# Performance work log

Measured on AMD Instinct MI355X. Metric: run time of the kernel, lower is better.

The kernel has to match this reference:

```python
import jax, jax.numpy as jnp
import numpy as np

C, H, G = 64, 8, 8
EPS = 1e-5


def setup_inputs() -> dict:
    key = jax.random.key(0)
    k1, k2, k3 = jax.random.split(key, 3)
    x = jax.random.normal(k1, (1, C, 16, 16, 16), dtype=jnp.float32)
    gn_weight = jnp.ones((C,), dtype=jnp.float32)
    gn_bias = jnp.zeros((C,), dtype=jnp.float32)
    qkv_w = jax.random.normal(k2, (3 * C, C), dtype=jnp.float32) * (C ** -0.5)
    out_w = jax.random.normal(k3, (C, C), dtype=jnp.float32) * (C ** -0.5)
    out_b = jnp.zeros((C,), dtype=jnp.float32)
    return {"x": x, "gn_weight": gn_weight, "gn_bias": gn_bias,
            "qkv_w": qkv_w, "out_w": out_w, "out_b": out_b}


def reference(x, gn_weight, gn_bias, qkv_w, out_w, out_b):
    B, Cc, X, Y, Z = x.shape
    D = Cc // H                     # head_dim
    S = X * Y * Z                   # flattened spatial length
    scale = D ** -0.5

    # GroupNorm over (C//G, X, Y, Z) per group
    xg = x.reshape(B, G, Cc // G, X, Y, Z)
    mu = xg.mean(axis=(2, 3, 4, 5), keepdims=True)
    var = xg.var(axis=(2, 3, 4, 5), keepdims=True)
    xn = ((xg - mu) * jax.lax.rsqrt(var + EPS)).reshape(B, Cc, X, Y, Z)
    xn = xn * gn_weight[None, :, None, None, None] + gn_bias[None, :, None, None, None]

    # 1x1x1 conv == channel matmul
    qkv = jnp.einsum('oc,bcxyz->boxyz', qkv_w, xn)
    q, k, v = jnp.split(qkv, 3, axis=1)            # each [B, C, X, Y, Z]
    q = q.reshape(B, H, D, S)
    k = k.reshape(B, H, D, S)
    v = v.reshape(B, H, D, S)

    scores = jnp.einsum('bhds,bhdt->bhst', q, k) * scale   # [B,H,S,S]
    probs = jax.nn.softmax(scores, axis=-1)
    out = jnp.einsum('bhst,bhdt->bhds', probs, v)          # [B,H,D,S]
    out = out.reshape(B, Cc, X, Y, Z)

    out = jnp.einsum('oc,bcxyz->boxyz', out_w, out) + out_b[None, :, None, None, None]
    return out + x
```

## Files before the change

kernel.cpp:

```cpp
#include <hip/hip_runtime.h>
#include <math.h>

#define S 4096
#define EPS 1e-5f

#if __has_builtin(__builtin_amdgcn_exp2f)
#define EXP2F(x) __builtin_amdgcn_exp2f(x)
#else
#define EXP2F(x) exp2f(x)
#endif

#define WS_PSUM 0
#define WS_PSQ  64
#define WS_ATT  16384
#define QT_B 1310720
#define KT_B 1835008
#define VB_B 2359296

typedef _Float16 h8_t __attribute__((ext_vector_type(8)));
typedef _Float16 h4_t __attribute__((ext_vector_type(4)));
typedef __fp16   fp16v2 __attribute__((ext_vector_type(2)));
typedef float    f4_t __attribute__((ext_vector_type(4)));

union H8 { h8_t h; int4 v; int i[4]; };
union H4 { h4_t h; int2 v; int i[2]; };

static __device__ __forceinline__ int pkrtz(float a, float b) {
    fp16v2 p = __builtin_amdgcn_cvt_pkrtz(a, b);
    union { fp16v2 h; int i; } u; u.h = p; return u.i;
}

__global__ __launch_bounds__(256) void k_gnstat1(const float* __restrict__ x,
                                                 float* __restrict__ ws) {
    int b = blockIdx.x;
    int tid = threadIdx.x;
    const float4* p = (const float4*)(x + b * 4096);
    float s = 0.f, sq = 0.f;
    #pragma unroll
    for (int i = 0; i < 4; ++i) {
        float4 v = p[tid + i * 256];
        s  += v.x + v.y + v.z + v.w;
        sq += v.x * v.x + v.y * v.y + v.z * v.z + v.w * v.w;
    }
    #pragma unroll
    for (int m = 32; m >= 1; m >>= 1) {
        s  += __shfl_xor(s, m);
        sq += __shfl_xor(sq, m);
    }
    __shared__ float ls[4], lq[4];
    int w = tid >> 6;
    if ((tid & 63) == 0) { ls[w] = s; lq[w] = sq; }
    __syncthreads();
    if (tid == 0) {
        ws[WS_PSUM + b] = ls[0] + ls[1] + ls[2] + ls[3];
        ws[WS_PSQ  + b] = lq[0] + lq[1] + lq[2] + lq[3];
    }
}

__global__ __launch_bounds__(256) void k_qkv(const float* __restrict__ x,
                                             const float* __restrict__ qkvw,
                                             const float* __restrict__ gnw,
                                             const float* __restrict__ gnb,
                                             float* __restrict__ ws) {
    __shared__ float la[64], lb2[64], lw[512], lbias[8];
    int tid = threadIdx.x;
    int o0 = blockIdx.y * 8;
    int s = blockIdx.x * 256 + tid;

    if (tid < 64) {
        float sm = ws[WS_PSUM + tid];
        float sq = ws[WS_PSQ + tid];
        #pragma unroll
        for (int m = 1; m < 8; m <<= 1) {
            sm += __shfl_xor(sm, m);
            sq += __shfl_xor(sq, m);
        }
        const float inv_n = 1.0f / 32768.0f;
        float mu  = sm * inv_n;
        float var = sq * inv_n - mu * mu;
        float rs  = rsqrtf(var + EPS);
        float a   = rs * gnw[tid];
        la[tid]  = a;
        lb2[tid] = gnb[tid] - mu * a;
    }
    __syncthreads();
    lw[tid]       = qkvw[o0 * 64 + tid]       * la[tid & 63];
    lw[tid + 256] = qkvw[o0 * 64 + 256 + tid] * la[tid & 63];
    {
        int wv = tid >> 6, ln = tid & 63;
        #pragma unroll
        for (int j = 0; j < 2; ++j) {
            int o = wv * 2 + j;
            float pb = qkvw[(o0 + o) * 64 + ln] * lb2[ln];
            #pragma unroll
            for (int m = 1; m < 64; m <<= 1) pb += __shfl_xor(pb, m);
            if (ln == 0) lbias[o] = pb;
        }
    }
    __syncthreads();

    float acc[8];
    #pragma unroll
    for (int o = 0; o < 8; ++o) acc[o] = lbias[o];
    for (int c = 0; c < 64; ++c) {
        float xv = x[c * S + s];
        #pragma unroll
        for (int o = 0; o < 8; ++o) acc[o] = fmaf(lw[o * 64 + c], xv, acc[o]);
    }

    char* base = (char*)ws;
    if (o0 < 64) {
        const float qsc = 0.51006776f;
        int hh = o0 >> 3;
        int4 r;
        r.x = pkrtz(acc[0] * qsc, acc[1] * qsc);
        r.y = pkrtz(acc[2] * qsc, acc[3] * qsc);
        r.z = pkrtz(acc[4] * qsc, acc[5] * qsc);
        r.w = pkrtz(acc[6] * qsc, acc[7] * qsc);
        *(int4*)(base + QT_B + (size_t)(hh * 4096 + s) * 16) = r;
    } else if (o0 < 128) {
        int hh = (o0 - 64) >> 3;
        int4 r;
        r.x = pkrtz(acc[0], acc[1]);
        r.y = pkrtz(acc[2], acc[3]);
        r.z = pkrtz(acc[4], acc[5]);
        r.w = pkrtz(acc[6], acc[7]);
        *(int4*)(base + KT_B + (size_t)(hh * 4096 + s) * 16) = r;
    } else {
        int hh = (o0 - 128) >> 3;
        _Float16* vb = (_Float16*)(base + VB_B);
        #pragma unroll
        for (int d = 0; d < 8; ++d)
            vb[(size_t)((hh * 8 + d) * 4096) + s] = (_Float16)acc[d];
    }
}

__global__ __launch_bounds__(512, 8) void k_attn(float* __restrict__ ws) {
    const int h = blockIdx.y;
    const int q0 = blockIdx.x * 32;
    const int tid = threadIdx.x;
    const int w = tid >> 6;
    const int lane = tid & 63;
    const int col = lane & 15;
    const int quad = lane >> 4;

    const char* base = (const char*)ws;
    const _Float16* Qt = (const _Float16*)(base + QT_B) + (size_t)h * 4096 * 8;
    const _Float16* Kt = (const _Float16*)(base + KT_B) + (size_t)h * 4096 * 8;
    const _Float16* Vb = (const _Float16*)(base + VB_B) + (size_t)h * 8 * 4096;

    __shared__ _Float16 Plds[8][2][16][40];
    __shared__ f4_t red[7][2][64];

    H4 qf0, qf1;
    qf0.i[0] = qf0.i[1] = 0;
    qf1 = qf0;
    if (quad < 2) {
        qf0.v = *(const int2*)(Qt + (size_t)(q0 + col) * 8 + quad * 4);
        qf1.v = *(const int2*)(Qt + (size_t)(q0 + 16 + col) * 8 + quad * 4);
    }

    H4 kf0, kf1;
    kf0.i[0] = kf0.i[1] = 0;
    kf1 = kf0;
    H8 vf;
    {
        int c8 = (col == 8) ? 0x3C003C00 : 0;
        vf.i[0] = c8; vf.i[1] = c8; vf.i[2] = c8; vf.i[3] = c8;
    }

    f4_t acc0 = {0.f, 0.f, 0.f, 0.f};
    f4_t acc1 = {0.f, 0.f, 0.f, 0.f};
    const f4_t z = {0.f, 0.f, 0.f, 0.f};
    _Float16* Prow0 = &Plds[w][0][0][0];
    _Float16* Prow1 = &Plds[w][1][0][0];

    const int tbase = w * 512;
    for (int it = 0; it < 16; ++it) {
        const int tt = tbase + it * 32;
        if (quad < 2) {
            kf0.v = *(const int2*)(Kt + (size_t)(tt + col) * 8 + quad * 4);
            kf1.v = *(const int2*)(Kt + (size_t)(tt + 16 + col) * 8 + quad * 4);
        }
        if (col < 8)
            vf.v = *(const int4*)(Vb + (size_t)col * 4096 + tt + quad * 8);

        f4_t s00 = __builtin_amdgcn_mfma_f32_16x16x16f16(kf0.h, qf0.h, z, 0, 0, 0);
        f4_t s01 = __builtin_amdgcn_mfma_f32_16x16x16f16(kf1.h, qf0.h, z, 0, 0, 0);
        f4_t s10 = __builtin_amdgcn_mfma_f32_16x16x16f16(kf0.h, qf1.h, z, 0, 0, 0);
        f4_t s11 = __builtin_amdgcn_mfma_f32_16x16x16f16(kf1.h, qf1.h, z, 0, 0, 0);

        #pragma unroll
        for (int r = 0; r < 4; ++r) {
            s00[r] = EXP2F(s00[r]); s01[r] = EXP2F(s01[r]);
            s10[r] = EXP2F(s10[r]); s11[r] = EXP2F(s11[r]);
        }

        int2 w0a = { pkrtz(s00[0], s00[1]), pkrtz(s00[2], s00[3]) };
        int2 w0b = { pkrtz(s01[0], s01[1]), pkrtz(s01[2], s01[3]) };
        *(int2*)(Prow0 + col * 40 + quad * 4)      = w0a;
        *(int2*)(Prow0 + col * 40 + 16 + quad * 4) = w0b;
        int2 w1a = { pkrtz(s10[0], s10[1]), pkrtz(s10[2], s10[3]) };
        int2 w1b = { pkrtz(s11[0], s11[1]), pkrtz(s11[2], s11[3]) };
        *(int2*)(Prow1 + col * 40 + quad * 4)      = w1a;
        *(int2*)(Prow1 + col * 40 + 16 + quad * 4) = w1b;

        H8 p0, p1;
        p0.v = *(const int4*)(Prow0 + col * 40 + quad * 8);
        p1.v = *(const int4*)(Prow1 + col * 40 + quad * 8);

        acc0 = __builtin_amdgcn_mfma_f32_16x16x32_f16(vf.h, p0.h, acc0, 0, 0, 0);
        acc1 = __builtin_amdgcn_mfma_f32_16x16x32_f16(vf.h, p1.h, acc1, 0, 0, 0);
    }

    if (w > 0) { red[w - 1][0][lane] = acc0; red[w - 1][1][lane] = acc1; }
    __syncthreads();
    if (w == 0) {
        #pragma unroll
        for (int r = 0; r < 7; ++r) {
            acc0 += red[r][0][lane];
            acc1 += red[r][1][lane];
        }
        float inv0 = 1.0f / __shfl(acc0[0], 32 + col, 64);
        float inv1 = 1.0f / __shfl(acc1[0], 32 + col, 64);
        if (quad < 2) {
            float* att = ws + WS_ATT + (size_t)(h * 8 + quad * 4) * S + q0;
            #pragma unroll
            for (int r = 0; r < 4; ++r) {
                att[r * S + col]      = acc0[r] * inv0;
                att[r * S + 16 + col] = acc1[r] * inv1;
            }
        }
    }
}

__global__ __launch_bounds__(256) void k_out(const float* __restrict__ x,
                                             const float* __restrict__ outw,
                                             const float* __restrict__ outb,
                                             const float* __restrict__ ws,
                                             float* __restrict__ out) {
    __shared__ float lw[512];
    __shared__ float lb[8];
    int tid = threadIdx.x;
    int o0 = blockIdx.y * 8;
    int s = blockIdx.x * 256 + tid;
    lw[tid]       = outw[o0 * 64 + tid];
    lw[tid + 256] = outw[o0 * 64 + 256 + tid];
    if (tid < 8) lb[tid] = outb[o0 + tid];
    __syncthreads();

    float acc[8];
    #pragma unroll
    for (int o = 0; o < 8; ++o) acc[o] = lb[o];
    const float* att = ws + WS_ATT;
    for (int c = 0; c < 64; ++c) {
        float av = att[c * S + s];
        #pragma unroll
        for (int o = 0; o < 8; ++o) acc[o] = fmaf(lw[o * 64 + c], av, acc[o]);
    }
    #pragma unroll
    for (int o = 0; o < 8; ++o)
        out[(o0 + o) * S + s] = acc[o] + x[(o0 + o) * S + s];
}

extern "C" void kernel_launch(void* const* d_in, const int* in_sizes, int n_in,
                              void* d_out, int out_size, void* d_ws, size_t ws_size,
                              hipStream_t stream) {
    const float* x    = (const float*)d_in[0];
    const float* gnw  = (const float*)d_in[1];
    const float* gnb  = (const float*)d_in[2];
    const float* qkvw = (const float*)d_in[3];
    const float* outw = (const float*)d_in[4];
    const float* outb = (const float*)d_in[5];
    float* out = (float*)d_out;
    float* ws  = (float*)d_ws;

    hipLaunchKernelGGL(k_gnstat1, dim3(64), dim3(256), 0, stream, x, ws);
    hipLaunchKernelGGL(k_qkv, dim3(16, 24), dim3(256), 0, stream, x, qkvw, gnw, gnb, ws);
    hipLaunchKernelGGL(k_attn, dim3(128, 8), dim3(512), 0, stream, ws);
    hipLaunchKernelGGL(k_out, dim3(16, 8), dim3(256), 0, stream, x, outw, outb, ws, out);
}
```

Baseline: 102.3 us.

## Use 32x32x16 MFMA for QK scores and prefetch next K/V tile

Replaces the four 16x16x16 MFMAs that computed a 32x32 score tile with a single 32x32x16 MFMA, loading full 8-half Q/K rows zero-padded in the upper lanes. The P tile layout in LDS is merged into one 32-row buffer written from the 32x32 accumulator layout. K and V fragments for the next iteration are loaded before the current compute, giving software prefetch. The aim is fewer MFMA issues and hidden global load latency, at the cost of extra registers for the prefetched fragments and 16-wide accumulators.

```diff
diff --git a/kernel.cpp b/kernel.cpp
--- a/kernel.cpp
+++ b/kernel.cpp
@@ -18,12 +18,11 @@
 #define VB_B 2359296
 
 typedef _Float16 h8_t __attribute__((ext_vector_type(8)));
-typedef _Float16 h4_t __attribute__((ext_vector_type(4)));
 typedef __fp16   fp16v2 __attribute__((ext_vector_type(2)));
-typedef float    f4_t __attribute__((ext_vector_type(4)));
+typedef float    f4_t  __attribute__((ext_vector_type(4)));
+typedef float    f16_t __attribute__((ext_vector_type(16)));
 
 union H8 { h8_t h; int4 v; int i[4]; };
-union H4 { h4_t h; int2 v; int i[2]; };
 
 static __device__ __forceinline__ int pkrtz(float a, float b) {
     fp16v2 p = __builtin_amdgcn_cvt_pkrtz(a, b);
@@ -141,76 +140,68 @@
     const int tid = threadIdx.x;
     const int w = tid >> 6;
     const int lane = tid & 63;
-    const int col = lane & 15;
+    const int col16 = lane & 15;
     const int quad = lane >> 4;
+    const int col32 = lane & 31;
+    const int half = lane >> 5;
 
     const char* base = (const char*)ws;
     const _Float16* Qt = (const _Float16*)(base + QT_B) + (size_t)h * 4096 * 8;
     const _Float16* Kt = (const _Float16*)(base + KT_B) + (size_t)h * 4096 * 8;
     const _Float16* Vb = (const _Float16*)(base + VB_B) + (size_t)h * 8 * 4096;
 
-    __shared__ _Float16 Plds[8][2][16][40];
+    __shared__ _Float16 Plds[8][32][40];
     __shared__ f4_t red[7][2][64];
 
-    H4 qf0, qf1;
-    qf0.i[0] = qf0.i[1] = 0;
-    qf1 = qf0;
-    if (quad < 2) {
-        qf0.v = *(const int2*)(Qt + (size_t)(q0 + col) * 8 + quad * 4);
-        qf1.v = *(const int2*)(Qt + (size_t)(q0 + 16 + col) * 8 + quad * 4);
-    }
-
-    H4 kf0, kf1;
-    kf0.i[0] = kf0.i[1] = 0;
-    kf1 = kf0;
+    H8 qf;
+    qf.i[0] = qf.i[1] = qf.i[2] = qf.i[3] = 0;
+    if (half == 0) qf.v = *(const int4*)(Qt + (size_t)(q0 + col32) * 8);
+
+    H8 kf;
+    kf.i[0] = kf.i[1] = kf.i[2] = kf.i[3] = 0;
     H8 vf;
     {
-        int c8 = (col == 8) ? 0x3C003C00 : 0;
+        int c8 = (col16 == 8) ? 0x3C003C00 : 0;
         vf.i[0] = c8; vf.i[1] = c8; vf.i[2] = c8; vf.i[3] = c8;
     }
+
+    const int tbase = w * 512;
+    if (half == 0) kf.v = *(const int4*)(Kt + (size_t)(tbase + col32) * 8);
+    if (col16 < 8) vf.v = *(const int4*)(Vb + (size_t)col16 * 4096 + tbase + quad * 8);
 
     f4_t acc0 = {0.f, 0.f, 0.f, 0.f};
     f4_t acc1 = {0.f, 0.f, 0.f, 0.f};
-    const f4_t z = {0.f, 0.f, 0.f, 0.f};
-    _Float16* Prow0 = &Plds[w][0][0][0];
-    _Float16* Prow1 = &Plds[w][1][0][0];
-
-    const int tbase = w * 512;
+    f16_t zc = {0.f, 0.f, 0.f, 0.f, 0.f, 0.f, 0.f, 0.f,
+                0.f, 0.f, 0.f, 0.f, 0.f, 0.f, 0.f, 0.f};
+    _Float16* Pw = &Plds[w][0][0];
+
     for (int it = 0; it < 16; ++it) {
-        const int tt = tbase + it * 32;
-        if (quad < 2) {
-            kf0.v = *(const int2*)(Kt + (size_t)(tt + col) * 8 + quad * 4);
-            kf1.v = *(const int2*)(Kt + (size_t)(tt + 16 + col) * 8 + quad * 4);
-        }
-        if (col < 8)
-            vf.v = *(const int4*)(Vb + (size_t)col * 4096 + tt + quad * 8);
-
-        f4_t s00 = __builtin_amdgcn_mfma_f32_16x16x16f16(kf0.h, qf0.h, z, 0, 0, 0);
-        f4_t s01 = __builtin_amdgcn_mfma_f32_16x16x16f16(kf1.h, qf0.h, z, 0, 0, 0);
-        f4_t s10 = __builtin_amdgcn_mfma_f32_16x16x16f16(kf0.h, qf1.h, z, 0, 0, 0);
-        f4_t s11 = __builtin_amdgcn_mfma_f32_16x16x16f16(kf1.h, qf1.h, z, 0, 0, 0);
-
-        #pragma unroll
-        for (int r = 0; r < 4; ++r) {
-            s00[r] = EXP2F(s00[r]); s01[r] = EXP2F(s01[r]);
-            s10[r] = EXP2F(s10[r]); s11[r] = EXP2F(s11[r]);
-        }
-
-        int2 w0a = { pkrtz(s00[0], s00[1]), pkrtz(s00[2], s00[3]) };
-        int2 w0b = { pkrtz(s01[0], s01[1]), pkrtz(s01[2], s01[3]) };
-        *(int2*)(Prow0 + col * 40 + quad * 4)      = w0a;
-        *(int2*)(Prow0 + col * 40 + 16 + quad * 4) = w0b;
-        int2 w1a = { pkrtz(s10[0], s10[1]), pkrtz(s10[2], s10[3]) };
-        int2 w1b = { pkrtz(s11[0], s11[1]), pkrtz(s11[2], s11[3]) };
-        *(int2*)(Prow1 + col * 40 + quad * 4)      = w1a;
-        *(int2*)(Prow1 + col * 40 + 16 + quad * 4) = w1b;
+        H8 nk = kf, nv = vf;
+        if (it < 15) {
+            const int tt = tbase + (it + 1) * 32;
+            if (half == 0) nk.v = *(const int4*)(Kt + (size_t)(tt + col32) * 8);
+            if (col16 < 8) nv.v = *(const int4*)(Vb + (size_t)col16 * 4096 + tt + quad * 8);
+        }
+
+        f16_t sc = __builtin_amdgcn_mfma_f32_32x32x16_f16(kf.h, qf.h, zc, 0, 0, 0);
+        #pragma unroll
+        for (int r = 0; r < 16; ++r) sc[r] = EXP2F(sc[r]);
+
+        #pragma unroll
+        for (int b = 0; b < 4; ++b) {
+            int2 wv = { pkrtz(sc[4 * b], sc[4 * b + 1]),
+                        pkrtz(sc[4 * b + 2], sc[4 * b + 3]) };
+            *(int2*)(Pw + col32 * 40 + 8 * b + 4 * half) = wv;
+        }
 
         H8 p0, p1;
-        p0.v = *(const int4*)(Prow0 + col * 40 + quad * 8);
-        p1.v = *(const int4*)(Prow1 + col * 40 + quad * 8);
+        p0.v = *(const int4*)(Pw + col16 * 40 + quad * 8);
+        p1.v = *(const int4*)(Pw + (col16 + 16) * 40 + quad * 8);
 
         acc0 = __builtin_amdgcn_mfma_f32_16x16x32_f16(vf.h, p0.h, acc0, 0, 0, 0);
         acc1 = __builtin_amdgcn_mfma_f32_16x16x32_f16(vf.h, p1.h, acc1, 0, 0, 0);
+
+        kf = nk; vf = nv;
     }
 
     if (w > 0) { red[w - 1][0][lane] = acc0; red[w - 1][1][lane] = acc1; }
@@ -221,14 +212,14 @@
             acc0 += red[r][0][lane];
             acc1 += red[r][1][lane];
         }
-        float inv0 = 1.0f / __shfl(acc0[0], 32 + col, 64);
-        float inv1 = 1.0f / __shfl(acc1[0], 32 + col, 64);
+        float inv0 = 1.0f / __shfl(acc0[0], 32 + col16, 64);
+        float inv1 = 1.0f / __shfl(acc1[0], 32 + col16, 64);
         if (quad < 2) {
             float* att = ws + WS_ATT + (size_t)(h * 8 + quad * 4) * S + q0;
             #pragma unroll
             for (int r = 0; r < 4; ++r) {
-                att[r * S + col]      = acc0[r] * inv0;
-                att[r * S + 16 + col] = acc1[r] * inv1;
+                att[r * S + col16]      = acc0[r] * inv0;
+                att[r * S + 16 + col16] = acc1[r] * inv1;
             }
         }
     }
```

Result: faster. 98.62 us (-3.6%).

## Feed exp scores directly from MFMA output registers into PV MFMA, dropping LDS staging

Applied to the files above, without the earlier changes.

Replaces the LDS round-trip used to transpose the P tile between the QK^T and PV matrix instructions. The key step shrinks to 16 per iteration so the 16x16x16 MFMA output layout can serve directly as the B operand of the next 16x16x16 MFMA. This removes the shared-memory writes and reads and the P buffer, but doubles the loop trip count and uses half-width MFMAs for the PV product. Loop unroll by 2 is added to compensate.

```diff
diff --git a/kernel.cpp b/kernel.cpp
--- a/kernel.cpp
+++ b/kernel.cpp
@@ -17,12 +17,10 @@
 #define KT_B 1835008
 #define VB_B 2359296
 
-typedef _Float16 h8_t __attribute__((ext_vector_type(8)));
 typedef _Float16 h4_t __attribute__((ext_vector_type(4)));
 typedef __fp16   fp16v2 __attribute__((ext_vector_type(2)));
-typedef float    f4_t __attribute__((ext_vector_type(4)));
-
-union H8 { h8_t h; int4 v; int i[4]; };
+typedef float    f4_t  __attribute__((ext_vector_type(4)));
+
 union H4 { h4_t h; int2 v; int i[2]; };
 
 static __device__ __forceinline__ int pkrtz(float a, float b) {
@@ -149,68 +147,48 @@
     const _Float16* Kt = (const _Float16*)(base + KT_B) + (size_t)h * 4096 * 8;
     const _Float16* Vb = (const _Float16*)(base + VB_B) + (size_t)h * 8 * 4096;
 
-    __shared__ _Float16 Plds[8][2][16][40];
     __shared__ f4_t red[7][2][64];
 
-    H4 qf0, qf1;
-    qf0.i[0] = qf0.i[1] = 0;
-    qf1 = qf0;
+    H4 q0f, q1f;
+    q0f.i[0] = q0f.i[1] = 0;
+    q1f = q0f;
     if (quad < 2) {
-        qf0.v = *(const int2*)(Qt + (size_t)(q0 + col) * 8 + quad * 4);
-        qf1.v = *(const int2*)(Qt + (size_t)(q0 + 16 + col) * 8 + quad * 4);
-    }
-
-    H4 kf0, kf1;
-    kf0.i[0] = kf0.i[1] = 0;
-    kf1 = kf0;
-    H8 vf;
+        q0f.v = *(const int2*)(Qt + (size_t)(q0 + col) * 8 + quad * 4);
+        q1f.v = *(const int2*)(Qt + (size_t)(q0 + 16 + col) * 8 + quad * 4);
+    }
+
+    H4 kf;
+    kf.i[0] = kf.i[1] = 0;
+    H4 vf;
     {
         int c8 = (col == 8) ? 0x3C003C00 : 0;
-        vf.i[0] = c8; vf.i[1] = c8; vf.i[2] = c8; vf.i[3] = c8;
+        vf.i[0] = c8; vf.i[1] = c8;
     }
 
     f4_t acc0 = {0.f, 0.f, 0.f, 0.f};
     f4_t acc1 = {0.f, 0.f, 0.f, 0.f};
     const f4_t z = {0.f, 0.f, 0.f, 0.f};
-    _Float16* Prow0 = &Plds[w][0][0][0];
-    _Float16* Prow1 = &Plds[w][1][0][0];
 
     const int tbase = w * 512;
-    for (int it = 0; it < 16; ++it) {
-        const int tt = tbase + it * 32;
-        if (quad < 2) {
-            kf0.v = *(const int2*)(Kt + (size_t)(tt + col) * 8 + quad * 4);
-            kf1.v = *(const int2*)(Kt + (size_t)(tt + 16 + col) * 8 + quad * 4);
-        }
+    #pragma unroll 2
+    for (int it = 0; it < 32; ++it) {
+        const int tt = tbase + it * 16;
+        if (quad < 2)
+            kf.v = *(const int2*)(Kt + (size_t)(tt + col) * 8 + quad * 4);
         if (col < 8)
-            vf.v = *(const int4*)(Vb + (size_t)col * 4096 + tt + quad * 8);
-
-        f4_t s00 = __builtin_amdgcn_mfma_f32_16x16x16f16(kf0.h, qf0.h, z, 0, 0, 0);
-        f4_t s01 = __builtin_amdgcn_mfma_f32_16x16x16f16(kf1.h, qf0.h, z, 0, 0, 0);
-        f4_t s10 = __builtin_amdgcn_mfma_f32_16x16x16f16(kf0.h, qf1.h, z, 0, 0, 0);
-        f4_t s11 = __builtin_amdgcn_mfma_f32_16x16x16f16(kf1.h, qf1.h, z, 0, 0, 0);
-
-        #pragma unroll
-        for (int r = 0; r < 4; ++r) {
-            s00[r] = EXP2F(s00[r]); s01[r] = EXP2F(s01[r]);
-            s10[r] = EXP2F(s10[r]); s11[r] = EXP2F(s11[r]);
-        }
-
-        int2 w0a = { pkrtz(s00[0], s00[1]), pkrtz(s00[2], s00[3]) };
-        int2 w0b = { pkrtz(s01[0], s01[1]), pkrtz(s01[2], s01[3]) };
-        *(int2*)(Prow0 + col * 40 + quad * 4)      = w0a;
-        *(int2*)(Prow0 + col * 40 + 16 + quad * 4) = w0b;
-        int2 w1a = { pkrtz(s10[0], s10[1]), pkrtz(s10[2], s10[3]) };
-        int2 w1b = { pkrtz(s11[0], s11[1]), pkrtz(s11[2], s11[3]) };
-        *(int2*)(Prow1 + col * 40 + quad * 4)      = w1a;
-        *(int2*)(Prow1 + col * 40 + 16 + quad * 4) = w1b;
-
-        H8 p0, p1;
-        p0.v = *(const int4*)(Prow0 + col * 40 + quad * 8);
-        p1.v = *(const int4*)(Prow1 + col * 40 + quad * 8);
-
-        acc0 = __builtin_amdgcn_mfma_f32_16x16x32_f16(vf.h, p0.h, acc0, 0, 0, 0);
-        acc1 = __builtin_amdgcn_mfma_f32_16x16x32_f16(vf.h, p1.h, acc1, 0, 0, 0);
+            vf.v = *(const int2*)(Vb + (size_t)col * 4096 + tt + quad * 4);
+
+        f4_t s0 = __builtin_amdgcn_mfma_f32_16x16x16f16(kf.h, q0f.h, z, 0, 0, 0);
+        f4_t s1 = __builtin_amdgcn_mfma_f32_16x16x16f16(kf.h, q1f.h, z, 0, 0, 0);
+
+        H4 p0, p1;
+        p0.i[0] = pkrtz(EXP2F(s0[0]), EXP2F(s0[1]));
+        p0.i[1] = pkrtz(EXP2F(s0[2]), EXP2F(s0[3]));
+        p1.i[0] = pkrtz(EXP2F(s1[0]), EXP2F(s1[1]));
+        p1.i[1] = pkrtz(EXP2F(s1[2]), EXP2F(s1[3]));
+
+        acc0 = __builtin_amdgcn_mfma_f32_16x16x16f16(vf.h, p0.h, acc0, 0, 0, 0);
+        acc1 = __builtin_amdgcn_mfma_f32_16x16x16f16(vf.h, p1.h, acc1, 0, 0, 0);
     }
 
     if (w > 0) { red[w - 1][0][lane] = acc0; red[w - 1][1][lane] = acc1; }
```

Measured after the change: 109.7 us. 1.07x slower.
